# Kernel tuning notes

Hardware: AMD Instinct MI355X
Metric: run time of the kernel (lower is better)

Reference implementation:

```python
import jax, jax.numpy as jnp
import numpy as np

jax.config.update('jax_enable_x64', True)

NV = 300000
NT = 1200000

# Lookup tables from GshellHelper buffers
TRIANGLE_TABLE = jnp.asarray(np.array([
    [-1, -1, -1, -1, -1, -1], [1, 0, 2, -1, -1, -1], [4, 0, 3, -1, -1, -1],
    [1, 4, 2, 1, 3, 4], [3, 1, 5, -1, -1, -1], [2, 3, 0, 2, 5, 3],
    [1, 4, 0, 1, 5, 4], [4, 2, 5, -1, -1, -1], [4, 5, 2, -1, -1, -1],
    [4, 1, 0, 4, 5, 1], [3, 2, 0, 3, 5, 2], [1, 3, 5, -1, -1, -1],
    [4, 1, 2, 4, 3, 1], [3, 0, 4, -1, -1, -1], [2, 0, 1, -1, -1, -1],
    [-1, -1, -1, -1, -1, -1]], dtype=np.int64))
NUM_TRIANGLES_TABLE = jnp.asarray(np.array([0, 1, 1, 2, 1, 2, 2, 1, 1, 2, 2, 1, 2, 1, 1, 0], dtype=np.int64))
BASE_TET_EDGES = jnp.asarray(np.array([0, 1, 0, 2, 0, 3, 1, 2, 1, 3, 2, 3], dtype=np.int64))


def setup_inputs() -> dict:
    key = jax.random.key(0)
    k1, k2, k3 = jax.random.split(key, 3)
    pos_nx3 = jax.random.normal(k1, (NV, 3), dtype=jnp.float32)
    sdf_n = jax.random.normal(k2, (NV,), dtype=jnp.float32)
    tet_fx4 = jax.random.randint(k3, (NT, 4), 0, NV, dtype=jnp.int64)
    return {'pos_nx3': pos_nx3, 'sdf_n': sdf_n, 'tet_fx4': tet_fx4}


def _marching_tets(pos_nx3, sdf_n, tet_fx4):
    Nv = pos_nx3.shape[0]
    Nt = tet_fx4.shape[0]
    U = Nt * 6  # max possible unique edges (padded, static)
    sentinel = Nv * Nv  # any real edge code is < Nv*Nv

    occ_n = sdf_n > 0                               # [Nv]
    occ_fx4 = occ_n[tet_fx4]                        # [Nt,4]

    # build the 6 edges of every tet and sort each pair (min, max)
    edges = tet_fx4[:, BASE_TET_EDGES].reshape(-1, 2)   # [Nt*6, 2]
    e0 = jnp.minimum(edges[:, 0], edges[:, 1])
    e1 = jnp.maximum(edges[:, 0], edges[:, 1])
    code = e0 * Nv + e1                                  # [Nt*6] int64 edge key

    # dedup edges (torch.unique(..., return_inverse=True) equivalent, padded)
    uniq, inv = jnp.unique(code, size=U, fill_value=sentinel, return_inverse=True)
    u0 = jnp.clip(uniq // Nv, 0, Nv - 1)
    u1 = jnp.clip(uniq % Nv, 0, Nv - 1)
    real = uniq < sentinel
    crossing = real & (occ_n[u0] != occ_n[u1])           # edges with a sign change

    # compacted index for crossing edges; -1 for non-crossing (as in torch mapping)
    mapping = jnp.where(crossing, jnp.cumsum(crossing.astype(jnp.int64)) - 1, -1)
    idx_map = mapping[inv].reshape(Nt, 6)                # [Nt,6]

    # linear interpolation to the zero crossing:
    # verts = (p0 * (-s1) + p1 * s0) / (s0 - s1)   (matches the torch flip/negate math)
    s0 = sdf_n[u0]
    s1 = sdf_n[u1]
    denom = jnp.where(crossing, s0 - s1, jnp.asarray(1.0, sdf_n.dtype))
    v = (pos_nx3[u0] * (-s1 / denom)[:, None] + pos_nx3[u1] * (s0 / denom)[:, None])

    # scatter interpolated verts to their compacted slots; drop non-crossing
    target = jnp.where(crossing, mapping, U)
    verts = jnp.zeros((U, 3), pos_nx3.dtype).at[target].set(v, mode='drop')

    # per-tet sign pattern -> triangle table lookup
    v_id = jnp.asarray([1, 2, 4, 8], dtype=jnp.int64)
    tetindex = (occ_fx4.astype(jnp.int64) * v_id[None, :]).sum(-1)   # [Nt]
    num_triangles = NUM_TRIANGLES_TABLE[tetindex]                     # [Nt] in {0,1,2}
    tri6 = TRIANGLE_TABLE[tetindex]                                   # [Nt,6]
    face_idx = jnp.take_along_axis(idx_map, jnp.clip(tri6, 0, 5), axis=1).reshape(Nt, 2, 3)
    valid_tri = jnp.arange(2, dtype=jnp.int64)[None, :] < num_triangles[:, None]
    faces = jnp.where(valid_tri[:, :, None], face_idx, -1)            # [Nt,2,3], -1 padded

    return verts, faces, num_triangles, crossing


def reference(pos_nx3, sdf_n, tet_fx4):
    return _marching_tets(pos_nx3, sdf_n, tet_fx4)
```

## Files before the change

### kernel.cpp

```cpp
#include <hip/hip_runtime.h>
#include <stdint.h>

typedef unsigned long long u64;
typedef unsigned int u32;

#define NVERT 300000
#define NTET  1200000
#define NE    (NTET*6)
#define TILE  4096
#define NTILES ((NE + TILE - 1)/TILE)
#define IDXBITS 23
#define IDXMASK ((1u<<IDXBITS)-1)
#define CODESHIFT 24
#define NBUCKS 4688
#define BUCKSHIFT 49

#define P1_TPB  1024
#define P1_KPT  32
#define P1_KEYS (P1_TPB*P1_KPT)
#define P1_GRID ((NE + P1_KEYS - 1)/P1_KEYS)

#define BSHIFT 16
#define BSZ    65536
#define NBUCK  110
#define BPB    8
#define STAGECAP 2240

#define VERTS_OFF 0
#define FACES_OFF 21600000
#define NUMT_OFF  28800000
#define CROSS_OFF 30000000
#define CODES_ELEM 14000000

__constant__ int c_ea[6] = {0,0,0,1,1,2};
__constant__ int c_eb[6] = {1,2,3,2,3,3};
__constant__ int c_numtri[16] = {0,1,1,2,1,2,2,1,1,2,2,1,2,1,1,0};
__constant__ int c_tritab[16][6] = {
 {-1,-1,-1,-1,-1,-1},{1,0,2,-1,-1,-1},{4,0,3,-1,-1,-1},{1,4,2,1,3,4},
 {3,1,5,-1,-1,-1},{2,3,0,2,5,3},{1,4,0,1,5,4},{4,2,5,-1,-1,-1},
 {4,5,2,-1,-1,-1},{4,1,0,4,5,1},{3,2,0,3,5,2},{1,3,5,-1,-1,-1},
 {4,1,2,4,3,1},{3,0,4,-1,-1,-1},{2,0,1,-1,-1,-1},{-1,-1,-1,-1,-1,-1}};

__device__ __forceinline__ int sw(int j){ return j ^ ((j >> 4) & 15); }

__global__ void k_pack(const int* __restrict__ tet, const float* __restrict__ sdf,
                       u64* __restrict__ dst, float* __restrict__ occF, u32* __restrict__ hist){
  __shared__ u32 h[NBUCKS];
  int tid = threadIdx.x;
  for (int r=tid; r<NBUCKS; r+=256) h[r]=0;
  __syncthreads();
  int t = blockIdx.x*blockDim.x + tid;
  if (t < NTET){
    int4 q = ((const int4*)tet)[t];
    int v[4] = {q.x, q.y, q.z, q.w};
    u32 o[4];
    int occ = 0;
    #pragma unroll
    for (int j=0;j<4;j++){ o[j] = sdf[v[j]] > 0.f ? 1u : 0u; occ |= (int)o[j] << j; }
    occF[t] = (float)occ;
    u64 base = (u64)t*6;
    #pragma unroll
    for (int k=0;k<6;k++){
      int a = v[c_ea[k]], b = v[c_eb[k]];
      u64 cross = (o[c_ea[k]] != o[c_eb[k]]) ? 1ull : 0ull;
      int e0 = min(a,b), e1 = max(a,b);
      u64 code = ((u64)e0 << 19) | (u64)e1;
      u64 key = (code << CODESHIFT) | (cross << IDXBITS) | (base + (u64)k);
      dst[base+k] = key;
      atomicAdd(&h[(u32)(key >> BUCKSHIFT)], 1u);
    }
  }
  __syncthreads();
  for (int r=tid; r<NBUCKS; r+=256){
    u32 c = h[r];
    if (c) atomicAdd(&hist[r], c);
  }
}

__global__ void k_psd(const float* __restrict__ pos, const float* __restrict__ sdf,
                      float4* __restrict__ psd){
  int v = blockIdx.x*blockDim.x + threadIdx.x;
  if (v < NVERT) psd[v] = make_float4(pos[3*v], pos[3*v+1], pos[3*v+2], sdf[v]);
}

__global__ void k_fillm1(float4* __restrict__ p, int n4){
  int i = blockIdx.x*blockDim.x + threadIdx.x;
  if (i < n4) p[i] = make_float4(-1.f,-1.f,-1.f,-1.f);
}

__global__ __launch_bounds__(1024) void k_scan_buckets(const u32* __restrict__ hist,
     u32* __restrict__ boff, u32* __restrict__ gcur){
  __shared__ u32 s[1024];
  int tid = threadIdx.x;
  u32 carry = 0;
  for (int start=0; start<NBUCKS; start+=1024){
    int idx = start + tid;
    u32 x = (idx < NBUCKS) ? hist[idx] : 0;
    s[tid] = x; __syncthreads();
    for (int off=1; off<1024; off<<=1){
      u32 t = (tid >= off) ? s[tid-off] : 0;
      __syncthreads();
      s[tid] += t;
      __syncthreads();
    }
    u32 excl = carry + s[tid] - x;
    if (idx < NBUCKS){ boff[idx] = excl; gcur[idx] = excl; }
    carry += s[1023];
    __syncthreads();
  }
}

__global__ __launch_bounds__(P1_TPB) void k_bucket_scatter(const u64* __restrict__ src,
     u64* __restrict__ dst, u32* __restrict__ gcur){
  __shared__ u32 h[NBUCKS];
  int tid = threadIdx.x;
  for (int r=tid;r<NBUCKS;r+=P1_TPB) h[r]=0;
  __syncthreads();
  size_t gi = (size_t)blockIdx.x*P1_KEYS + (size_t)tid*P1_KPT;
  u64 kk[P1_KPT];
  if (gi + P1_KPT <= NE){
    const ulonglong2* p2 = (const ulonglong2*)(src + gi);
    #pragma unroll
    for (int k2=0;k2<P1_KPT/2;k2++){ ulonglong2 t = p2[k2]; kk[2*k2]=t.x; kk[2*k2+1]=t.y; }
  } else {
    #pragma unroll
    for (int k=0;k<P1_KPT;k++) kk[k] = (gi+k < NE) ? src[gi+k] : ~0ull;
  }
  #pragma unroll
  for (int k=0;k<P1_KPT;k++){
    if (gi+k < NE) atomicAdd(&h[(u32)(kk[k] >> BUCKSHIFT)], 1u);
  }
  __syncthreads();
  for (int r=tid;r<NBUCKS;r+=P1_TPB){
    u32 c = h[r];
    h[r] = c ? atomicAdd(&gcur[r], c) : 0u;
  }
  __syncthreads();
  #pragma unroll
  for (int k=0;k<P1_KPT;k++){
    if (gi+k < NE){
      u32 b = (u32)(kk[k] >> BUCKSHIFT);
      u32 p = atomicAdd(&h[b], 1u);
      dst[p] = kk[k];
    }
  }
}

template<int NK>
__global__ __launch_bounds__(256) void k_sort_bucket(const u64* __restrict__ src,
     u64* __restrict__ dst, const u32* __restrict__ hist, const u32* __restrict__ boff){
  __shared__ u64 keys[NK*256];
  __shared__ u64 wsum[4][2];
  int b = blockIdx.x, tid = threadIdx.x;
  u32 n = hist[b];
  if (n == 0) return;
  if (NK == 4  && n > 1024) return;
  if (NK == 8  && (n <= 1024 || n > 2048)) return;
  if (NK == 16 && n <= 2048) return;
  u32 base = boff[b];
  #pragma unroll
  for (int k=0;k<NK;k++){
    int j = k*256 + tid;
    keys[sw(j)] = (j < (int)n) ? src[base + j] : ~0ull;
  }
  __syncthreads();
  int mywave = tid >> 6;
  #pragma unroll 1
  for (int q=0;q<9;q++){
    int sh = 24 + 3*q;
    u64 myk[NK];
    u64 vpack = 0;
    u64 c0 = 0, c1 = 0;
    #pragma unroll
    for (int k=0;k<NK;k++){
      myk[k] = keys[sw(tid*NK+k)];
      u32 d = (u32)((myk[k] >> sh) & 7);
      vpack |= (u64)d << (3*k);
      u64 inc = 1ull << (16*(d&3));
      c0 += (d & 4) ? 0 : inc;
      c1 += (d & 4) ? inc : 0;
    }
    u64 v0 = c0, v1 = c1;
    #pragma unroll
    for (int off=1; off<64; off<<=1){
      u64 t0 = __shfl_up(v0, off, 64);
      u64 t1 = __shfl_up(v1, off, 64);
      if ((tid & 63) >= off){ v0 += t0; v1 += t1; }
    }
    if ((tid & 63) == 63){ wsum[mywave][0] = v0; wsum[mywave][1] = v1; }
    __syncthreads();
    u64 pre0=0, pre1=0, tot0=0, tot1=0;
    #pragma unroll
    for (int wv=0; wv<4; wv++){
      u64 x0 = wsum[wv][0], x1 = wsum[wv][1];
      if (wv < mywave){ pre0 += x0; pre1 += x1; }
      tot0 += x0; tot1 += x1;
    }
    u64 run0 = v0 + pre0 - c0;
    u64 run1 = v1 + pre1 - c1;
    u64 Bp0 = 0, Bp1 = 0;
    u32 acc = 0;
    #pragma unroll
    for (int b2=0;b2<8;b2++){
      u32 f = (u32)(((b2 < 4 ? tot0 : tot1) >> (16*(b2&3))) & 0xFFFF);
      if (b2 < 4) Bp0 |= (u64)acc << (16*b2);
      else        Bp1 |= (u64)acc << (16*(b2&3));
      acc += f;
    }
    #pragma unroll
    for (int k=0;k<NK;k++){
      u32 d = (u32)((vpack >> (3*k)) & 7);
      u32 s2 = d & 3;
      bool hi = (d & 4) != 0;
      u64 Bsel = hi ? Bp1 : Bp0;
      u64 rsel = hi ? run1 : run0;
      u32 pos = (u32)((Bsel >> (16*s2)) & 0xFFFF) + (u32)((rsel >> (16*s2)) & 0xFFFF);
      u64 inc = 1ull << (16*s2);
      run0 += hi ? 0 : inc;
      run1 += hi ? inc : 0;
      keys[sw((int)pos)] = myk[k];
    }
    __syncthreads();
  }
  #pragma unroll
  for (int k=0;k<NK;k++){
    int j = k*256 + tid;
    if (j < (int)n) dst[base + j] = keys[sw(j)];
  }
}

__global__ __launch_bounds__(256) void k_tilesum(const u64* __restrict__ A, u64* __restrict__ tileSums){
  __shared__ u64 s[256];
  int tid = threadIdx.x;
  int start = blockIdx.x*TILE + tid*16;
  u64 myk[16];
  if (start < NE){
    const ulonglong2* A2 = (const ulonglong2*)(A + start);
    #pragma unroll
    for (int k2=0;k2<8;k2++){ ulonglong2 t = A2[k2]; myk[2*k2]=t.x; myk[2*k2+1]=t.y; }
  } else {
    #pragma unroll
    for (int k=0;k<16;k++) myk[k]=0;
  }
  u64 prev = (start > 0 && start <= NE) ? A[start-1] : ~0ull;
  u32 th=0, tc=0;
  #pragma unroll
  for (int k=0;k<16;k++){
    int i = start + k;
    if (i < NE){
      u64 v = myk[k];
      if ((v>>CODESHIFT) != (prev>>CODESHIFT)){
        th++;
        if ((v>>IDXBITS) & 1ull) tc++;
      }
      prev = v;
    }
  }
  s[tid] = ((u64)th<<32) | (u64)tc;
  __syncthreads();
  for (int off=128; off>0; off>>=1){
    if (tid<off) s[tid]+=s[tid+off];
    __syncthreads();
  }
  if (tid==0) tileSums[blockIdx.x] = s[0];
}

__global__ void k_scan_tiles(u64* __restrict__ tileSums, u64* __restrict__ tileOff){
  __shared__ u64 s[256];
  int tid = threadIdx.x;
  u64 carry=0;
  for (int start=0; start<NTILES; start+=256){
    int idx=start+tid;
    u64 x = (idx<NTILES)? tileSums[idx] : 0;
    s[tid]=x; __syncthreads();
    for (int off=1;off<256;off<<=1){
      u64 t=(tid>=off)?s[tid-off]:0;
      __syncthreads();
      s[tid]+=t;
      __syncthreads();
    }
    u64 incl=s[tid], tot=s[255];
    if (idx<NTILES) tileOff[idx] = carry + incl - x;
    carry += tot;
    __syncthreads();
  }
  if (tid==0) tileOff[NTILES] = carry;
}

__global__ __launch_bounds__(256) void k_emit_light(const u64* __restrict__ A,
     const u64* __restrict__ tileOff, u64* __restrict__ pairs, u32* __restrict__ cursors,
     u64* __restrict__ codes, float* __restrict__ crossing_out){
  __shared__ u64 s[256];
  __shared__ u32 cnt[NBUCK], lcur[NBUCK];
  __shared__ u32 lofs[NBUCK+1];
  __shared__ u32 gbase[NBUCK];
  __shared__ u32 pscan[128];
  __shared__ u64 stage[STAGECAP];
  int tid=threadIdx.x, blk=blockIdx.x;
  int start = blk*TILE + tid*16;
  if (tid < NBUCK){ cnt[tid]=0; lcur[tid]=0; }
  u64 myk[16];
  if (start < NE){
    const ulonglong2* A2 = (const ulonglong2*)(A + start);
    #pragma unroll
    for (int k2=0;k2<8;k2++){ ulonglong2 t = A2[k2]; myk[2*k2]=t.x; myk[2*k2+1]=t.y; }
  } else {
    #pragma unroll
    for (int k=0;k<16;k++) myk[k]=0;
  }
  u64 prev = (start > 0 && start <= NE) ? A[start-1] : ~0ull;
  u32 headm=0, crossm=0;
  #pragma unroll
  for (int k=0;k<16;k++){
    int i = start + k;
    if (i<NE){
      u64 v = myk[k];
      if ((v>>CODESHIFT) != (prev>>CODESHIFT)) headm |= 1u<<k;
      if ((v>>IDXBITS) & 1ull) crossm |= 1u<<k;
      prev = v;
    }
  }
  __syncthreads();
  #pragma unroll
  for (int k=0;k<16;k++){
    if ((start+k) < NE && ((crossm>>k)&1u))
      atomicAdd(&cnt[((u32)myk[k] & IDXMASK)>>BSHIFT], 1u);
  }
  u32 th = __popc(headm), tc = __popc(headm & crossm);
  u64 x = ((u64)th<<32)|(u64)tc;
  s[tid]=x; __syncthreads();
  for (int off=1;off<256;off<<=1){
    u64 t=(tid>=off)?s[tid-off]:0;
    __syncthreads();
    s[tid]+=t;
    __syncthreads();
  }
  u64 excl = s[tid]-x;
  if (tid < 128) pscan[tid] = (tid < NBUCK) ? cnt[tid] : 0;
  __syncthreads();
  for (int off=1; off<128; off<<=1){
    u32 t = 0;
    if (tid < 128 && tid >= off) t = pscan[tid-off];
    __syncthreads();
    if (tid < 128) pscan[tid] += t;
    __syncthreads();
  }
  if (tid < NBUCK) lofs[tid] = pscan[tid] - cnt[tid];
  if (tid == 0) lofs[NBUCK] = pscan[127];
  if (tid < NBUCK) gbase[tid] = atomicAdd(&cursors[tid], cnt[tid]);
  __syncthreads();
  bool use_stage = (lofs[NBUCK] <= STAGECAP);
  u64 baseOff = tileOff[blk] + excl;
  u32 H = (u32)(baseOff>>32);
  u32 C = (u32)(baseOff & 0xFFFFFFFFull);
  #pragma unroll
  for (int k=0;k<16;k++){
    int i = start+k;
    if (i>=NE) break;
    bool head  = (headm>>k)&1u;
    bool cross = (crossm>>k)&1u;
    if (head){ H++; if(cross) C++; }
    if (cross){
      int m = (int)C-1;
      u32 orig = (u32)myk[k] & IDXMASK;
      u32 b = orig>>BSHIFT;
      u32 r = atomicAdd(&lcur[b], 1u);
      u64 pr = ((u64)orig<<32) | (u64)(u32)m;
      if (use_stage) stage[lofs[b] + r] = pr;
      else           pairs[(size_t)b*BSZ + gbase[b] + r] = pr;
    }
    if (head){
      crossing_out[H-1] = cross ? 1.f : 0.f;
      if (cross) codes[C-1] = myk[k]>>CODESHIFT;
    }
  }
  __syncthreads();
  if (use_stage){
    int ncross = (int)lofs[NBUCK];
    for (int j = tid; j < ncross; j += 256){
      int lo=0, hi=NBUCK;
      while (hi - lo > 1){ int mid=(lo+hi)>>1; if ((int)lofs[mid] <= j) lo=mid; else hi=mid; }
      pairs[(size_t)lo*BSZ + gbase[lo] + (u32)(j - (int)lofs[lo])] = stage[j];
    }
  }
}

__global__ __launch_bounds__(256) void k_verts(const u64* __restrict__ codes,
     const float4* __restrict__ psd, const u64* __restrict__ totptr, float* __restrict__ verts){
  __shared__ u64 dummy[5120];
  u32 ncross = (u32)(totptr[0] & 0xFFFFFFFFull);
  u32 stride = gridDim.x * blockDim.x;
  for (u32 i = blockIdx.x*blockDim.x + threadIdx.x; i < ncross; i += stride){
    u64 code = codes[i];
    u32 u0 = (u32)(code >> 19), u1 = (u32)(code & 0x7FFFFull);
    float4 a = psd[u0], b = psd[u1];
    float denom = a.w - b.w;
    float w0 = (-b.w)/denom, w1 = a.w/denom;
    verts[3*i+0] = a.x*w0 + b.x*w1;
    verts[3*i+1] = a.y*w0 + b.y*w1;
    verts[3*i+2] = a.z*w0 + b.z*w1;
  }
  if ((int)ncross < -1){ dummy[threadIdx.x] = codes[0]; verts[0] = (float)dummy[255]; }
}

__global__ void k_map_scatter(const u64* __restrict__ pairs, const u32* __restrict__ cursors,
                              float* __restrict__ mapF){
  int b = blockIdx.x / BPB, sub = blockIdx.x % BPB;
  u32 n = cursors[b];
  const u64* p = pairs + (size_t)b*BSZ;
  for (u32 i = (u32)(sub*256 + threadIdx.x); i < n; i += BPB*256){
    u64 v = p[i];
    mapF[(u32)(v>>32)] = (float)(int)(u32)v;
  }
}

__global__ void k_faces(const float* __restrict__ occF, float* faceRegion, float* __restrict__ numt){
  int t = blockIdx.x*blockDim.x + threadIdx.x;
  if (t>=NTET) return;
  int occ = (int)occF[t];
  int ntri = c_numtri[occ];
  float em[6];
  #pragma unroll
  for (int j=0;j<6;j++) em[j] = faceRegion[t*6+j];
  float f[6];
  #pragma unroll
  for (int j=0;j<6;j++){
    int tri = c_tritab[occ][j];
    f[j] = ((j/3) < ntri) ? em[tri] : -1.f;
  }
  #pragma unroll
  for (int j=0;j<6;j++) faceRegion[t*6+j] = f[j];
  numt[t] = (float)ntri;
}

extern "C" void kernel_launch(void* const* d_in, const int* in_sizes, int n_in,
                              void* d_out, int out_size, void* d_ws, size_t ws_size,
                              hipStream_t stream) {
  const float* pos = (const float*)d_in[0];
  const float* sdf = (const float*)d_in[1];
  const int*   tet = (const int*)d_in[2];
  float* out = (float*)d_out;

  char* w = (char*)d_ws;
  u64* bufA     = (u64*)w;
  u32* hist     = (u32*)(w + 57600000);
  u32* boff     = (u32*)(w + 57618752);
  u32* gcur     = (u32*)(w + 57637504);
  u64* tileSums = (u64*)(w + 57656256);
  u64* tileOff  = (u64*)(w + 57670320);
  u32* cursors  = (u32*)(w + 57684392);
  float4* psd   = (float4*)(w + 57684992);
  u64* pairs_ws = (u64*)(w + 62484992);

  u64* bufB  = (u64*)d_out;
  u64* codes = (u64*)(out + CODES_ELEM);

  hipMemsetAsync(hist, 0, NBUCKS*sizeof(u32), stream);

  k_pack<<<(NTET+255)/256, 256, 0, stream>>>(tet, sdf, bufA, out + NUMT_OFF, hist);
  k_psd<<<(NVERT+255)/256, 256, 0, stream>>>(pos, sdf, psd);
  k_fillm1<<<(7200000/4 + 255)/256, 256, 0, stream>>>((float4*)(out + FACES_OFF), 7200000/4);

  k_scan_buckets<<<1, 1024, 0, stream>>>(hist, boff, gcur);

  k_bucket_scatter<<<P1_GRID, P1_TPB, 0, stream>>>(bufA, bufB, gcur);
  k_sort_bucket<4><<<NBUCKS, 256, 0, stream>>>(bufB, bufA, hist, boff);
  k_sort_bucket<8><<<NBUCKS, 256, 0, stream>>>(bufB, bufA, hist, boff);
  k_sort_bucket<16><<<NBUCKS, 256, 0, stream>>>(bufB, bufA, hist, boff);

  k_tilesum<<<NTILES, 256, 0, stream>>>(bufA, tileSums);
  k_scan_tiles<<<1, 256, 0, stream>>>(tileSums, tileOff);

  hipMemsetAsync(out + CROSS_OFF, 0, (size_t)7200000*4, stream);
  hipMemsetAsync(cursors, 0, NBUCK*sizeof(u32), stream);

  k_emit_light<<<NTILES, 256, 0, stream>>>(bufA, tileOff, pairs_ws, cursors,
                                           codes, out + CROSS_OFF);

  hipMemsetAsync(out + VERTS_OFF, 0, (size_t)CODES_ELEM*4, stream);
  k_verts<<<1024, 256, 0, stream>>>(codes, psd, tileOff + NTILES, out + VERTS_OFF);
  hipMemsetAsync(out + CODES_ELEM, 0, (size_t)(21600000-CODES_ELEM)*4, stream);

  k_map_scatter<<<NBUCK*BPB, 256, 0, stream>>>(pairs_ws, cursors, out + FACES_OFF);
  k_faces<<<(NTET+255)/256, 256, 0, stream>>>(out + NUMT_OFF, out + FACES_OFF, out + NUMT_OFF);
}
```

Baseline: 607.1 us.

## Use persistent pack with per-block histograms and zero only output tails

k_pack becomes a grid-stride kernel with a fixed grid. Each block stages its keys in shared memory and writes them out coalesced. It stores a private histogram row instead of doing global atomics, and a new small kernel sums those rows. The full-region memsets of the verts and crossing outputs are replaced by one kernel that zeroes only the part past the live counts. This cuts redundant output writes and global atomic traffic, at the cost of an extra reduction launch and a pack grid that may be less parallel.

```diff
diff --git a/kernel.cpp b/kernel.cpp
--- a/kernel.cpp
+++ b/kernel.cpp
@@ -15,6 +15,8 @@
 #define NBUCKS 4688
 #define BUCKSHIFT 49
 
+#define PK_GRID 512
+
 #define P1_TPB  1024
 #define P1_KPT  32
 #define P1_KEYS (P1_TPB*P1_KPT)
@@ -43,38 +45,51 @@
 
 __device__ __forceinline__ int sw(int j){ return j ^ ((j >> 4) & 15); }
 
-__global__ void k_pack(const int* __restrict__ tet, const float* __restrict__ sdf,
-                       u64* __restrict__ dst, float* __restrict__ occF, u32* __restrict__ hist){
+__global__ __launch_bounds__(256) void k_pack(const int* __restrict__ tet, const float* __restrict__ sdf,
+                       u64* __restrict__ dst, float* __restrict__ occF, u32* __restrict__ histBlk){
   __shared__ u32 h[NBUCKS];
+  __shared__ u64 lk[256*6];
   int tid = threadIdx.x;
   for (int r=tid; r<NBUCKS; r+=256) h[r]=0;
   __syncthreads();
-  int t = blockIdx.x*blockDim.x + tid;
-  if (t < NTET){
-    int4 q = ((const int4*)tet)[t];
-    int v[4] = {q.x, q.y, q.z, q.w};
-    u32 o[4];
-    int occ = 0;
-    #pragma unroll
-    for (int j=0;j<4;j++){ o[j] = sdf[v[j]] > 0.f ? 1u : 0u; occ |= (int)o[j] << j; }
-    occF[t] = (float)occ;
-    u64 base = (u64)t*6;
-    #pragma unroll
-    for (int k=0;k<6;k++){
-      int a = v[c_ea[k]], b = v[c_eb[k]];
-      u64 cross = (o[c_ea[k]] != o[c_eb[k]]) ? 1ull : 0ull;
-      int e0 = min(a,b), e1 = max(a,b);
-      u64 code = ((u64)e0 << 19) | (u64)e1;
-      u64 key = (code << CODESHIFT) | (cross << IDXBITS) | (base + (u64)k);
-      dst[base+k] = key;
-      atomicAdd(&h[(u32)(key >> BUCKSHIFT)], 1u);
-    }
-  }
-  __syncthreads();
-  for (int r=tid; r<NBUCKS; r+=256){
-    u32 c = h[r];
-    if (c) atomicAdd(&hist[r], c);
-  }
+  for (int t0 = blockIdx.x*256; t0 < NTET; t0 += PK_GRID*256){
+    int t = t0 + tid;
+    if (t < NTET){
+      int4 q = ((const int4*)tet)[t];
+      int v[4] = {q.x, q.y, q.z, q.w};
+      u32 o[4];
+      int occ = 0;
+      #pragma unroll
+      for (int j=0;j<4;j++){ o[j] = sdf[v[j]] > 0.f ? 1u : 0u; occ |= (int)o[j] << j; }
+      occF[t] = (float)occ;
+      u64 base = (u64)t*6;
+      #pragma unroll
+      for (int k=0;k<6;k++){
+        int a = v[c_ea[k]], b = v[c_eb[k]];
+        u64 cross = (o[c_ea[k]] != o[c_eb[k]]) ? 1ull : 0ull;
+        int e0 = min(a,b), e1 = max(a,b);
+        u64 code = ((u64)e0 << 19) | (u64)e1;
+        u64 key = (code << CODESHIFT) | (cross << IDXBITS) | (base + (u64)k);
+        lk[tid*6+k] = key;
+        atomicAdd(&h[(u32)(key >> BUCKSHIFT)], 1u);
+      }
+    }
+    __syncthreads();
+    int nt = NTET - t0; if (nt > 256) nt = 256;
+    size_t ob = (size_t)t0*6;
+    for (int j=tid; j<nt*6; j+=256) dst[ob + j] = lk[j];
+    __syncthreads();
+  }
+  u32* row = histBlk + (size_t)blockIdx.x * NBUCKS;
+  for (int r=tid; r<NBUCKS; r+=256) row[r] = h[r];
+}
+
+__global__ void k_reduce_hist(const u32* __restrict__ histBlk, u32* __restrict__ hist){
+  int b = blockIdx.x*256 + threadIdx.x;
+  if (b >= NBUCKS) return;
+  u32 s = 0;
+  for (int r=0;r<PK_GRID;r++) s += histBlk[(size_t)r*NBUCKS + b];
+  hist[b] = s;
 }
 
 __global__ void k_psd(const float* __restrict__ pos, const float* __restrict__ sdf,
@@ -403,6 +418,21 @@
   if ((int)ncross < -1){ dummy[threadIdx.x] = codes[0]; verts[0] = (float)dummy[255]; }
 }
 
+__global__ void k_tailzero(const u64* __restrict__ totptr,
+                           float* __restrict__ verts, float* __restrict__ cross){
+  u64 tot = totptr[0];
+  u32 nuniq  = (u32)(tot>>32);
+  u32 ncross = (u32)(tot & 0xFFFFFFFFull);
+  u32 vstart = 3u*ncross;
+  u32 vlen = 21600000u - vstart;
+  u32 clen = 7200000u - nuniq;
+  u32 stride = gridDim.x * blockDim.x;
+  for (u32 i = blockIdx.x*blockDim.x + threadIdx.x; i < vlen; i += stride)
+    verts[vstart + i] = 0.f;
+  for (u32 i = blockIdx.x*blockDim.x + threadIdx.x; i < clen; i += stride)
+    cross[nuniq + i] = 0.f;
+}
+
 __global__ void k_map_scatter(const u64* __restrict__ pairs, const u32* __restrict__ cursors,
                               float* __restrict__ mapF){
   int b = blockIdx.x / BPB, sub = blockIdx.x % BPB;
@@ -451,16 +481,16 @@
   u32* cursors  = (u32*)(w + 57684392);
   float4* psd   = (float4*)(w + 57684992);
   u64* pairs_ws = (u64*)(w + 62484992);
+  u32* histBlk  = (u32*)pairs_ws;
 
   u64* bufB  = (u64*)d_out;
   u64* codes = (u64*)(out + CODES_ELEM);
 
-  hipMemsetAsync(hist, 0, NBUCKS*sizeof(u32), stream);
-
-  k_pack<<<(NTET+255)/256, 256, 0, stream>>>(tet, sdf, bufA, out + NUMT_OFF, hist);
+  k_pack<<<PK_GRID, 256, 0, stream>>>(tet, sdf, bufA, out + NUMT_OFF, histBlk);
   k_psd<<<(NVERT+255)/256, 256, 0, stream>>>(pos, sdf, psd);
   k_fillm1<<<(7200000/4 + 255)/256, 256, 0, stream>>>((float4*)(out + FACES_OFF), 7200000/4);
 
+  k_reduce_hist<<<(NBUCKS+255)/256, 256, 0, stream>>>(histBlk, hist);
   k_scan_buckets<<<1, 1024, 0, stream>>>(hist, boff, gcur);
 
   k_bucket_scatter<<<P1_GRID, P1_TPB, 0, stream>>>(bufA, bufB, gcur);
@@ -471,15 +501,13 @@
   k_tilesum<<<NTILES, 256, 0, stream>>>(bufA, tileSums);
   k_scan_tiles<<<1, 256, 0, stream>>>(tileSums, tileOff);
 
-  hipMemsetAsync(out + CROSS_OFF, 0, (size_t)7200000*4, stream);
   hipMemsetAsync(cursors, 0, NBUCK*sizeof(u32), stream);
 
   k_emit_light<<<NTILES, 256, 0, stream>>>(bufA, tileOff, pairs_ws, cursors,
                                            codes, out + CROSS_OFF);
 
-  hipMemsetAsync(out + VERTS_OFF, 0, (size_t)CODES_ELEM*4, stream);
   k_verts<<<1024, 256, 0, stream>>>(codes, psd, tileOff + NTILES, out + VERTS_OFF);
-  hipMemsetAsync(out + CODES_ELEM, 0, (size_t)(21600000-CODES_ELEM)*4, stream);
+  k_tailzero<<<2048, 256, 0, stream>>>(tileOff + NTILES, out + VERTS_OFF, out + CROSS_OFF);
 
   k_map_scatter<<<NBUCK*BPB, 256, 0, stream>>>(pairs_ws, cursors, out + FACES_OFF);
   k_faces<<<(NTET+255)/256, 256, 0, stream>>>(out + NUMT_OFF, out + FACES_OFF, out + NUMT_OFF);
```

Measured after the change: 526.1 us. 13.3% less time.
